# Performance work log

Hardware: AMD Instinct MI355X
Metric: run time of the kernel (lower is better)

The kernel has to match this reference:

```python
import jax, jax.numpy as jnp
import numpy as np
from jax import lax

# Module constraint: hidden_dim == state_dim == expand_dim (see broadcasting in original).
H = 128  # hidden_dim
N = 128  # state_dim
E = 128  # expand_dim = hidden_dim * expand_factor (expand_factor=1)
B, L = 4, 1024


def setup_inputs() -> dict:
    key = jax.random.key(0)
    ks = jax.random.split(key, 11)
    s = lambda fan: 1.0 / np.sqrt(fan)
    return {
        "u": jax.random.normal(ks[0], (B, L, H), jnp.float32),
        "W_in": jax.random.normal(ks[1], (H, 2 * E), jnp.float32) * s(H),
        "b_in": jax.random.normal(ks[2], (2 * E,), jnp.float32) * 0.01,
        "conv_w": jax.random.normal(ks[3], (E, 1, 3), jnp.float32) * s(3),
        "conv_b": jax.random.normal(ks[4], (E,), jnp.float32) * 0.01,
        "W_x": jax.random.normal(ks[5], (E, N + N + H), jnp.float32) * s(E),
        "b_x": jax.random.normal(ks[6], (N + N + H,), jnp.float32) * 0.01,
        "A_log": jax.random.normal(ks[7], (N,), jnp.float32),
        "D": jnp.ones((H,), jnp.float32),
        "W_out": jax.random.normal(ks[8], (E, H), jnp.float32) * s(E),
        "b_out": jax.random.normal(ks[9], (H,), jnp.float32) * 0.01,
    }


def reference(u, W_in, b_in, conv_w, conv_b, W_x, b_x, A_log, D, W_out, b_out):
    b, l, _ = u.shape
    xz = u @ W_in + b_in                       # [B,L,2E]
    x, z = jnp.split(xz, 2, axis=-1)           # [B,L,E] each
    # depthwise conv1d, kernel 3, padding 1 (groups == channels)
    xc = lax.conv_general_dilated(
        x.transpose(0, 2, 1), conv_w, window_strides=(1,), padding=[(1, 1)],
        feature_group_count=E, dimension_numbers=("NCH", "OIH", "NCH"))
    x = jax.nn.silu(xc.transpose(0, 2, 1) + conv_b)  # [B,L,E]
    ssm = x @ W_x + b_x                        # [B,L,2N+H]
    delta = jax.nn.softplus(ssm[..., :N])      # [B,L,N]
    Bm = ssm[..., N:2 * N]                     # [B,L,N]
    C = ssm[..., 2 * N:]                       # [B,L,H]
    A = -jnp.exp(A_log)                        # [N]

    def step(h, inp):
        d_t, B_t, C_t, x_t, u_t = inp          # [B,N],[B,N],[B,H],[B,E],[B,H]
        # A_discrete[b,t,i,j] = exp(delta[b,t,i] * A[j])  (outer broadcast, as in source)
        A_disc = jnp.exp(d_t[:, :, None] * A[None, None, :])       # [B,N,N]
        h = A_disc * h + (d_t * B_t)[:, :, None] * x_t[:, None, :]  # [B,N,E]
        y = (h * C_t[:, None, :]).sum(axis=1) + D * u_t             # [B,H]
        return h, y

    h0 = jnp.zeros((b, N, H), u.dtype)
    inputs = (delta.transpose(1, 0, 2), Bm.transpose(1, 0, 2),
              C.transpose(1, 0, 2), x.transpose(1, 0, 2), u.transpose(1, 0, 2))
    _, ys = lax.scan(step, h0, inputs)         # ys: [L,B,H]
    y = ys.transpose(1, 0, 2) * jax.nn.silu(z)  # [B,L,H] (E==H)
    return y @ W_out + b_out                   # dropout in eval mode: identity
```

## Files before the change

### kernel.cpp

```cpp
#include <hip/hip_runtime.h>
#include <hip/hip_bf16.h>

using bf16 = __hip_bfloat16;
typedef __attribute__((ext_vector_type(8))) short short8;
typedef __attribute__((ext_vector_type(4))) float f32x4;

#define BVAL 4
#define LVAL 1024
#define LOG2E 1.44269504f

#define TSEG 64
#define SSEG 16
#define JW 8
#define CH 16
#define PTS3 76

#define OFF_BIN    0
#define OFF_CONVW  256
#define OFF_CONVB  640
#define OFF_BX     768
#define OFF_ALOG   1152
#define OFF_D      1280
#define OFF_BOUT   1408
#define CVT_SMALL  1536

#define R_UBF   524288
#define R_WTIN  (R_UBF + 32768)
#define R_WTX   (R_WTIN + 49152)
#define R_WTOUT (R_WTX + 16384)
#define R_TOT   (R_WTOUT + CVT_SMALL)

__device__ __forceinline__ int dtype_flag(const void* D) {
    return ((*(const unsigned int*)D) & 0xFFFFu) != 0u ? 1 : 0;
}
__device__ __forceinline__ float ldin(const void* p, size_t i, int f) {
    return f ? __bfloat162float(((const bf16*)p)[i]) : ((const float*)p)[i];
}
__device__ __forceinline__ short f2bf(float x) {
    union { bf16 h; short s; } u; u.h = __float2bfloat16(x); return u.s;
}

__global__ void k0_cvt(const void* __restrict__ u, const void* __restrict__ W_in,
                       const void* __restrict__ b_in, const void* __restrict__ conv_w,
                       const void* __restrict__ conv_b, const void* __restrict__ W_x,
                       const void* __restrict__ b_x, const void* __restrict__ A_log,
                       const void* __restrict__ D, const void* __restrict__ W_out,
                       const void* __restrict__ b_out,
                       float* __restrict__ cvt, bf16* __restrict__ ubf,
                       bf16* __restrict__ wtin, bf16* __restrict__ wtx,
                       bf16* __restrict__ wtout) {
    int idx = blockIdx.x * 256 + threadIdx.x;
    if (idx >= R_TOT) return;
    int f = dtype_flag(D);
    if (idx < R_UBF) {
        ubf[idx] = __float2bfloat16(ldin(u, idx, f));
    } else if (idx < R_WTIN) {
        int rel = idx - R_UBF; int n = rel >> 7, k = rel & 127;
        wtin[rel] = __float2bfloat16(ldin(W_in, (size_t)k * 256 + n, f));
    } else if (idx < R_WTX) {
        int rel = idx - R_WTIN; int n = rel >> 7, k = rel & 127;
        wtx[rel] = __float2bfloat16(ldin(W_x, (size_t)k * 384 + n, f));
    } else if (idx < R_WTOUT) {
        int rel = idx - R_WTX; int n = rel >> 7, k = rel & 127;
        wtout[rel] = __float2bfloat16(ldin(W_out, (size_t)k * 128 + n, f));
    } else {
        int rel = idx - R_WTOUT; const void* p; int loc;
        if      (rel < 256)  { p = b_in;   loc = rel; }
        else if (rel < 640)  { p = conv_w; loc = rel - 256; }
        else if (rel < 768)  { p = conv_b; loc = rel - 640; }
        else if (rel < 1152) { p = b_x;    loc = rel - 768; }
        else if (rel < 1280) { p = A_log;  loc = rel - 1152; }
        else if (rel < 1408) { p = D;      loc = rel - 1280; }
        else                 { p = b_out;  loc = rel - 1408; }
        cvt[rel] = ldin(p, loc, f);
    }
}

__global__ void k1_mfma(const bf16* __restrict__ ubf, const bf16* __restrict__ wtin,
                        const float* __restrict__ cvt,
                        float* __restrict__ x_pre, float* __restrict__ zs) {
    int blk = blockIdx.x, mb = blk >> 3, cb = blk & 7;
    int tid = threadIdx.x, w = tid >> 6, lane = tid & 63;
    int quad = lane >> 4, sub = lane & 15;
    int m0 = mb * 64 + w * 16, c = cb * 16;
    f32x4 accX = {0.f, 0.f, 0.f, 0.f}, accZ = {0.f, 0.f, 0.f, 0.f};
    #pragma unroll
    for (int ks = 0; ks < 4; ++ks) {
        int k0 = ks * 32 + quad * 8;
        short8 a  = *(const short8*)(ubf + (size_t)(m0 + sub) * 128 + k0);
        short8 bX = *(const short8*)(wtin + (size_t)(c + sub) * 128 + k0);
        short8 bZ = *(const short8*)(wtin + (size_t)(128 + c + sub) * 128 + k0);
        accX = __builtin_amdgcn_mfma_f32_16x16x32_bf16(a, bX, accX, 0, 0, 0);
        accZ = __builtin_amdgcn_mfma_f32_16x16x32_bf16(a, bZ, accZ, 0, 0, 0);
    }
    int o = c + sub;
    float bx_ = cvt[OFF_BIN + o], bz_ = cvt[OFF_BIN + 128 + o];
    #pragma unroll
    for (int r = 0; r < 4; ++r) {
        int m = m0 + quad * 4 + r;
        float x = accX[r] + bx_;
        float z = accZ[r] + bz_;
        x_pre[(size_t)m * 128 + o] = x;
        zs[(size_t)m * 128 + o] = z / (1.0f + __expf(-z));
    }
}

__global__ void k3_mfma(const float* __restrict__ x_pre, const bf16* __restrict__ wtx,
                        const float* __restrict__ cvt, float* __restrict__ xs,
                        float* __restrict__ delta, float* __restrict__ dB,
                        float* __restrict__ Cc) {
    __shared__ float swc[128 * 4];
    int blk = blockIdx.x, mb = blk >> 3, cb = blk & 7;
    int tid = threadIdx.x, w = tid >> 6, lane = tid & 63;
    int quad = lane >> 4, sub = lane & 15;
    if (tid < 128) {
        swc[tid * 4 + 0] = cvt[OFF_CONVW + tid * 3 + 0];
        swc[tid * 4 + 1] = cvt[OFF_CONVW + tid * 3 + 1];
        swc[tid * 4 + 2] = cvt[OFF_CONVW + tid * 3 + 2];
        swc[tid * 4 + 3] = cvt[OFF_CONVB + tid];
    }
    __syncthreads();
    int m0 = mb * 64 + w * 16, c = cb * 16;
    int row = m0 + sub;
    int l = row & (LVAL - 1);
    const float* xr = x_pre + (size_t)row * 128;
    f32x4 accA = {0.f,0.f,0.f,0.f}, accB = {0.f,0.f,0.f,0.f}, accC = {0.f,0.f,0.f,0.f};
    #pragma unroll
    for (int ks = 0; ks < 4; ++ks) {
        int k0 = ks * 32 + quad * 8;
        float ccv[8], mmv[8], ppv[8];
        *(float4*)&ccv[0] = *(const float4*)(xr + k0);
        *(float4*)&ccv[4] = *(const float4*)(xr + k0 + 4);
        if (l > 0) {
            *(float4*)&mmv[0] = *(const float4*)(xr + k0 - 128);
            *(float4*)&mmv[4] = *(const float4*)(xr + k0 - 124);
        } else {
            #pragma unroll
            for (int i = 0; i < 8; ++i) mmv[i] = 0.f;
        }
        if (l < LVAL - 1) {
            *(float4*)&ppv[0] = *(const float4*)(xr + k0 + 128);
            *(float4*)&ppv[4] = *(const float4*)(xr + k0 + 132);
        } else {
            #pragma unroll
            for (int i = 0; i < 8; ++i) ppv[i] = 0.f;
        }
        float o[8];
        short8 a;
        #pragma unroll
        for (int i = 0; i < 8; ++i) {
            const float* wc = &swc[(k0 + i) * 4];
            float v = fmaf(wc[0], mmv[i], fmaf(wc[1], ccv[i], fmaf(wc[2], ppv[i], wc[3])));
            o[i] = v / (1.0f + __expf(-v));
            a[i] = f2bf(o[i]);
        }
        if (cb == 0) {
            *(float4*)(xs + (size_t)row * 128 + k0)     = *(float4*)&o[0];
            *(float4*)(xs + (size_t)row * 128 + k0 + 4) = *(float4*)&o[4];
        }
        short8 bA = *(const short8*)(wtx + (size_t)(c + sub) * 128 + k0);
        short8 bB = *(const short8*)(wtx + (size_t)(128 + c + sub) * 128 + k0);
        short8 bC = *(const short8*)(wtx + (size_t)(256 + c + sub) * 128 + k0);
        accA = __builtin_amdgcn_mfma_f32_16x16x32_bf16(a, bA, accA, 0, 0, 0);
        accB = __builtin_amdgcn_mfma_f32_16x16x32_bf16(a, bB, accB, 0, 0, 0);
        accC = __builtin_amdgcn_mfma_f32_16x16x32_bf16(a, bC, accC, 0, 0, 0);
    }
    int o = c + sub;
    float ba = cvt[OFF_BX + o], bb = cvt[OFF_BX + 128 + o], bc = cvt[OFF_BX + 256 + o];
    #pragma unroll
    for (int r = 0; r < 4; ++r) {
        int m = m0 + quad * 4 + r;
        size_t idx = (size_t)m * 128 + o;
        float d = accA[r] + ba;
        float sp = (d > 20.0f) ? d : log1pf(__expf(d));
        delta[idx] = sp;
        dB[idx] = sp * (accB[r] + bb);
        Cc[idx] = accC[r] + bc;
    }
}

__global__ __launch_bounds__(512, 8)
void k5a(const float* __restrict__ cvt, const float* __restrict__ delta,
         const float* __restrict__ dB, const float* __restrict__ xs,
         float* __restrict__ hout, float* __restrict__ Sd) {
    __shared__ float sdl[CH * 128], swl[CH * 128];
    __shared__ float sx[TSEG][JW];
    int blk = blockIdx.x;
    int b = blk >> 8, s = (blk >> 4) & 15, jg = blk & 15;
    int tid = threadIdx.x, w = tid >> 6, lane = tid & 63;
    int j = jg * JW + w;
    int t0 = s * TSEG;
    size_t base = (size_t)b * LVAL * 128;
    {
        int tt = tid >> 3, jj = tid & 7;
        sx[tt][jj] = xs[base + (size_t)(t0 + tt) * 128 + jg * JW + jj];
    }
    float a2 = -__expf(cvt[OFF_ALOG + j]) * LOG2E;
    float h0 = 0.f, h1 = 0.f, sd0 = 0.f, sd1 = 0.f;
    const float4* gd4 = (const float4*)(delta + base);
    const float4* gw4 = (const float4*)(dB + base);
    for (int c4 = 0; c4 < TSEG / CH; ++c4) {
        __syncthreads();
        int fb = (t0 + c4 * CH) * 32;
        ((float4*)sdl)[tid] = gd4[fb + tid];
        ((float4*)swl)[tid] = gw4[fb + tid];
        __syncthreads();
        #pragma unroll 8
        for (int k = 0; k < CH; ++k) {
            float2 dd = *(const float2*)&sdl[k * 128 + 2 * lane];
            float2 ww = *(const float2*)&swl[k * 128 + 2 * lane];
            float e0 = exp2f(dd.x * a2), e1 = exp2f(dd.y * a2);
            float xv = sx[c4 * CH + k][w];
            h0 = fmaf(e0, h0, ww.x * xv);
            h1 = fmaf(e1, h1, ww.y * xv);
            sd0 += dd.x; sd1 += dd.y;
        }
    }
    size_t cidx = (((size_t)(b * SSEG + s) * 128 + j) * 128) + 2 * lane;
    *(float2*)(hout + cidx) = make_float2(h0, h1);
    if (jg == 0 && w == 0) {
        *(float2*)(Sd + (size_t)(b * SSEG + s) * 128 + 2 * lane) = make_float2(sd0, sd1);
    }
}

__global__ void k5b(const float* __restrict__ cvt, const float* __restrict__ hout,
                    const float* __restrict__ Sd, float* __restrict__ hin) {
    int c = blockIdx.x * 2 + (threadIdx.x >> 6);
    int lane = threadIdx.x & 63;
    int b = c >> 7, j = c & 127;
    float a2 = -__expf(cvt[OFF_ALOG + j]) * LOG2E;
    float h0 = 0.f, h1 = 0.f;
    #pragma unroll
    for (int s = 0; s < SSEG; ++s) {
        size_t idx = (((size_t)(b * SSEG + s) * 128 + j) * 128) + 2 * lane;
        *(float2*)(hin + idx) = make_float2(h0, h1);
        float2 ho = *(const float2*)(hout + idx);
        float2 sd = *(const float2*)(Sd + (size_t)(b * SSEG + s) * 128 + 2 * lane);
        h0 = fmaf(exp2f(a2 * sd.x), h0, ho.x);
        h1 = fmaf(exp2f(a2 * sd.y), h1, ho.y);
    }
}

__global__ __launch_bounds__(512, 8)
void k5c(const float* __restrict__ cvt, const float* __restrict__ delta,
         const float* __restrict__ dB, const float* __restrict__ Cc,
         const float* __restrict__ xs, const float* __restrict__ zs,
         const float* __restrict__ hin, const void* __restrict__ uin,
         const void* __restrict__ Din, bf16* __restrict__ y2bf) {
    __shared__ float sdl[CH * 128], swl[CH * 128];
    __shared__ float sx[TSEG][JW];
    __shared__ float pt[JW][8 * PTS3];
    int blk = blockIdx.x;
    int b = blk >> 8, s = (blk >> 4) & 15, jg = blk & 15;
    int tid = threadIdx.x, w = tid >> 6, lane = tid & 63;
    int j = jg * JW + w;
    int t0 = s * TSEG;
    size_t base = (size_t)b * LVAL * 128;
    int f = dtype_flag(Din);
    {
        int tt = tid >> 3, jj = tid & 7;
        sx[tt][jj] = xs[base + (size_t)(t0 + tt) * 128 + jg * JW + jj];
    }
    float a2 = -__expf(cvt[OFF_ALOG + j]) * LOG2E;
    float Dj = cvt[OFF_D + j];
    size_t cidx = (((size_t)(b * SSEG + s) * 128 + j) * 128) + 2 * lane;
    float2 hh = *(const float2*)(hin + cidx);
    float h0 = hh.x, h1 = hh.y;
    const float4* gd4 = (const float4*)(delta + base);
    const float4* gw4 = (const float4*)(dB + base);
    float* ptw = pt[w];
    int t_r = lane >> 3, g8 = lane & 7;
    for (int c4 = 0; c4 < TSEG / CH; ++c4) {
        __syncthreads();
        int fb = (t0 + c4 * CH) * 32;
        ((float4*)sdl)[tid] = gd4[fb + tid];
        ((float4*)swl)[tid] = gw4[fb + tid];
        __syncthreads();
        for (int cb = 0; cb < CH / 8; ++cb) {
            int tte = c4 * CH + cb * 8 + t_r;
            size_t gi = base + (size_t)(t0 + tte) * 128 + j;
            float cC = Cc[gi];
            float cz = zs[gi];
            float cu = ldin(uin, gi, f);
            #pragma unroll
            for (int k = 0; k < 8; ++k) {
                int kk = cb * 8 + k;
                float2 dd = *(const float2*)&sdl[kk * 128 + 2 * lane];
                float2 ww = *(const float2*)&swl[kk * 128 + 2 * lane];
                float xv = sx[c4 * CH + kk][w];
                h0 = fmaf(exp2f(dd.x * a2), h0, ww.x * xv);
                h1 = fmaf(exp2f(dd.y * a2), h1, ww.y * xv);
                ptw[k * PTS3 + lane] = h0 + h1;
            }
            const float4* pr = (const float4*)&ptw[t_r * PTS3 + g8 * 8];
            float4 v0 = pr[0], v1 = pr[1];
            float sum = ((v0.x + v0.y) + (v0.z + v0.w)) + ((v1.x + v1.y) + (v1.z + v1.w));
            sum += __shfl_xor(sum, 1, 64);
            sum += __shfl_xor(sum, 2, 64);
            sum += __shfl_xor(sum, 4, 64);
            if (g8 == 0) {
                float y = fmaf(cC, sum, Dj * cu);
                y2bf[gi] = __float2bfloat16(y * cz);
            }
        }
    }
}

__global__ void k6_mfma(const bf16* __restrict__ y2bf, const bf16* __restrict__ wtout,
                        const float* __restrict__ cvt, const void* __restrict__ Din,
                        void* __restrict__ out) {
    int blk = blockIdx.x, mb = blk >> 2, nb = blk & 3;
    int tid = threadIdx.x, w = tid >> 6, lane = tid & 63;
    int quad = lane >> 4, sub = lane & 15;
    int m0 = mb * 64 + w * 16, n0 = nb * 32;
    f32x4 acc0 = {0.f,0.f,0.f,0.f}, acc1 = {0.f,0.f,0.f,0.f};
    #pragma unroll
    for (int ks = 0; ks < 4; ++ks) {
        int k0 = ks * 32 + quad * 8;
        short8 a  = *(const short8*)(y2bf + (size_t)(m0 + sub) * 128 + k0);
        short8 b0 = *(const short8*)(wtout + (size_t)(n0 + sub) * 128 + k0);
        short8 b1 = *(const short8*)(wtout + (size_t)(n0 + 16 + sub) * 128 + k0);
        acc0 = __builtin_amdgcn_mfma_f32_16x16x32_bf16(a, b0, acc0, 0, 0, 0);
        acc1 = __builtin_amdgcn_mfma_f32_16x16x32_bf16(a, b1, acc1, 0, 0, 0);
    }
    int f = dtype_flag(Din);
    float bo0 = cvt[OFF_BOUT + n0 + sub], bo1 = cvt[OFF_BOUT + n0 + 16 + sub];
    #pragma unroll
    for (int r = 0; r < 4; ++r) {
        int m = m0 + quad * 4 + r;
        float v0 = acc0[r] + bo0, v1 = acc1[r] + bo1;
        if (f) {
            ((bf16*)out)[(size_t)m * 128 + n0 + sub] = __float2bfloat16(v0);
            ((bf16*)out)[(size_t)m * 128 + n0 + 16 + sub] = __float2bfloat16(v1);
        } else {
            ((float*)out)[(size_t)m * 128 + n0 + sub] = v0;
            ((float*)out)[(size_t)m * 128 + n0 + 16 + sub] = v1;
        }
    }
}

extern "C" void kernel_launch(void* const* d_in, const int* in_sizes, int n_in,
                              void* d_out, int out_size, void* d_ws, size_t ws_size,
                              hipStream_t stream) {
    const size_t NE = (size_t)BVAL * LVAL * 128;
    const size_t NC = (size_t)BVAL * SSEG * 128 * 128;

    float* cvt   = (float*)d_ws;
    float* bufs  = cvt + 2048;
    float* x_pre = bufs + 0 * NE;
    float* zs    = bufs + 1 * NE;
    float* xs    = bufs + 2 * NE;
    float* delta = bufs + 3 * NE;
    float* dB    = bufs + 4 * NE;
    float* Cc    = bufs + 5 * NE;
    float* hout  = bufs + 6 * NE;
    float* hin   = hout + NC;
    float* Sd    = hin + NC;
    bf16* ubf    = (bf16*)(Sd + 8192);
    bf16* y2bf   = ubf + NE;
    bf16* wtin   = y2bf + NE;
    bf16* wtx    = wtin + 32768;
    bf16* wtout  = wtx + 49152;

    k0_cvt<<<(R_TOT + 255) / 256, 256, 0, stream>>>(
        d_in[0], d_in[1], d_in[2], d_in[3], d_in[4], d_in[5],
        d_in[6], d_in[7], d_in[8], d_in[9], d_in[10],
        cvt, ubf, wtin, wtx, wtout);
    k1_mfma<<<512, 256, 0, stream>>>(ubf, wtin, cvt, x_pre, zs);
    k3_mfma<<<512, 256, 0, stream>>>(x_pre, wtx, cvt, xs, delta, dB, Cc);
    k5a<<<BVAL * SSEG * (128 / JW), 512, 0, stream>>>(cvt, delta, dB, xs, hout, Sd);
    k5b<<<256, 128, 0, stream>>>(cvt, hout, Sd, hin);
    k5c<<<BVAL * SSEG * (128 / JW), 512, 0, stream>>>(cvt, delta, dB, Cc, xs, zs, hin,
        d_in[0], d_in[8], y2bf);
    k6_mfma<<<256, 256, 0, stream>>>(y2bf, wtout, cvt, d_in[8], d_out);
}
```

Before: 153.2 us.

## Replace chunked three-pass scan with single sequential scan split over state halves

Replaces the three-kernel segmented scan (local scan, carry propagation, rescan with output) with one sequential scan kernel over the full sequence. Each block handles one batch and 8 columns for half of the state dimension, with double-buffered prefetch of delta/dB/x into shared memory. Per-half partial C·h sums go to two buffers, and the D*u skip term, gating by z and the bf16 cast move into the output GEMM's A-operand load. This removes the second scan pass and the carry kernel, but leaves only 128 blocks, each running a 1024-step serial chain.

```diff
diff --git a/kernel.cpp b/kernel.cpp
--- a/kernel.cpp
+++ b/kernel.cpp
@@ -9,11 +9,9 @@
 #define LVAL 1024
 #define LOG2E 1.44269504f
 
-#define TSEG 64
-#define SSEG 16
-#define JW 8
-#define CH 16
-#define PTS3 76
+#define SCH 16
+#define NCHUNK (LVAL / SCH)
+#define PTS 68
 
 #define OFF_BIN    0
 #define OFF_CONVW  256
@@ -179,151 +177,116 @@
     }
 }
 
-__global__ __launch_bounds__(512, 8)
-void k5a(const float* __restrict__ cvt, const float* __restrict__ delta,
-         const float* __restrict__ dB, const float* __restrict__ xs,
-         float* __restrict__ hout, float* __restrict__ Sd) {
-    __shared__ float sdl[CH * 128], swl[CH * 128];
-    __shared__ float sx[TSEG][JW];
+__global__ __launch_bounds__(512)
+void k5_scan(const float* __restrict__ cvt, const float* __restrict__ delta,
+             const float* __restrict__ dB, const float* __restrict__ xs,
+             const float* __restrict__ Cc, float* __restrict__ pP0) {
+    __shared__ float sd[2][SCH][64];
+    __shared__ float sw[2][SCH][64];
+    __shared__ float sxc[2][SCH][8];
+    __shared__ float spt[8][8 * PTS];
+    const size_t NEc = (size_t)BVAL * LVAL * 128;
     int blk = blockIdx.x;
-    int b = blk >> 8, s = (blk >> 4) & 15, jg = blk & 15;
+    int half = blk & 1, jg = (blk >> 1) & 15, b = blk >> 5;
     int tid = threadIdx.x, w = tid >> 6, lane = tid & 63;
-    int j = jg * JW + w;
-    int t0 = s * TSEG;
+    int j = jg * 8 + w;
     size_t base = (size_t)b * LVAL * 128;
-    {
-        int tt = tid >> 3, jj = tid & 7;
-        sx[tt][jj] = xs[base + (size_t)(t0 + tt) * 128 + jg * JW + jj];
-    }
+    float* __restrict__ pP = pP0 + (size_t)half * NEc;
     float a2 = -__expf(cvt[OFF_ALOG + j]) * LOG2E;
-    float h0 = 0.f, h1 = 0.f, sd0 = 0.f, sd1 = 0.f;
     const float4* gd4 = (const float4*)(delta + base);
     const float4* gw4 = (const float4*)(dB + base);
-    for (int c4 = 0; c4 < TSEG / CH; ++c4) {
-        __syncthreads();
-        int fb = (t0 + c4 * CH) * 32;
-        ((float4*)sdl)[tid] = gd4[fb + tid];
-        ((float4*)swl)[tid] = gw4[fb + tid];
-        __syncthreads();
-        #pragma unroll 8
-        for (int k = 0; k < CH; ++k) {
-            float2 dd = *(const float2*)&sdl[k * 128 + 2 * lane];
-            float2 ww = *(const float2*)&swl[k * 128 + 2 * lane];
-            float e0 = exp2f(dd.x * a2), e1 = exp2f(dd.y * a2);
-            float xv = sx[c4 * CH + k][w];
-            h0 = fmaf(e0, h0, ww.x * xv);
-            h1 = fmaf(e1, h1, ww.y * xv);
-            sd0 += dd.x; sd1 += dd.y;
-        }
-    }
-    size_t cidx = (((size_t)(b * SSEG + s) * 128 + j) * 128) + 2 * lane;
-    *(float2*)(hout + cidx) = make_float2(h0, h1);
-    if (jg == 0 && w == 0) {
-        *(float2*)(Sd + (size_t)(b * SSEG + s) * 128 + 2 * lane) = make_float2(sd0, sd1);
-    }
-}
-
-__global__ void k5b(const float* __restrict__ cvt, const float* __restrict__ hout,
-                    const float* __restrict__ Sd, float* __restrict__ hin) {
-    int c = blockIdx.x * 2 + (threadIdx.x >> 6);
-    int lane = threadIdx.x & 63;
-    int b = c >> 7, j = c & 127;
-    float a2 = -__expf(cvt[OFF_ALOG + j]) * LOG2E;
-    float h0 = 0.f, h1 = 0.f;
-    #pragma unroll
-    for (int s = 0; s < SSEG; ++s) {
-        size_t idx = (((size_t)(b * SSEG + s) * 128 + j) * 128) + 2 * lane;
-        *(float2*)(hin + idx) = make_float2(h0, h1);
-        float2 ho = *(const float2*)(hout + idx);
-        float2 sd = *(const float2*)(Sd + (size_t)(b * SSEG + s) * 128 + 2 * lane);
-        h0 = fmaf(exp2f(a2 * sd.x), h0, ho.x);
-        h1 = fmaf(exp2f(a2 * sd.y), h1, ho.y);
-    }
-}
-
-__global__ __launch_bounds__(512, 8)
-void k5c(const float* __restrict__ cvt, const float* __restrict__ delta,
-         const float* __restrict__ dB, const float* __restrict__ Cc,
-         const float* __restrict__ xs, const float* __restrict__ zs,
-         const float* __restrict__ hin, const void* __restrict__ uin,
-         const void* __restrict__ Din, bf16* __restrict__ y2bf) {
-    __shared__ float sdl[CH * 128], swl[CH * 128];
-    __shared__ float sx[TSEG][JW];
-    __shared__ float pt[JW][8 * PTS3];
-    int blk = blockIdx.x;
-    int b = blk >> 8, s = (blk >> 4) & 15, jg = blk & 15;
-    int tid = threadIdx.x, w = tid >> 6, lane = tid & 63;
-    int j = jg * JW + w;
-    int t0 = s * TSEG;
-    size_t base = (size_t)b * LVAL * 128;
-    int f = dtype_flag(Din);
+    int st = (tid & 255) >> 4, sq = tid & 15;
     {
-        int tt = tid >> 3, jj = tid & 7;
-        sx[tt][jj] = xs[base + (size_t)(t0 + tt) * 128 + jg * JW + jj];
-    }
-    float a2 = -__expf(cvt[OFF_ALOG + j]) * LOG2E;
-    float Dj = cvt[OFF_D + j];
-    size_t cidx = (((size_t)(b * SSEG + s) * 128 + j) * 128) + 2 * lane;
-    float2 hh = *(const float2*)(hin + cidx);
-    float h0 = hh.x, h1 = hh.y;
-    const float4* gd4 = (const float4*)(delta + base);
-    const float4* gw4 = (const float4*)(dB + base);
-    float* ptw = pt[w];
+        float4 v;
+        if (tid < 256) v = gd4[st * 32 + half * 16 + sq];
+        else           v = gw4[st * 32 + half * 16 + sq];
+        if (tid < 256) *(float4*)&sd[0][st][sq * 4] = v;
+        else           *(float4*)&sw[0][st][sq * 4] = v;
+        if (tid < 128) sxc[0][tid >> 3][tid & 7] =
+            xs[base + (size_t)(tid >> 3) * 128 + jg * 8 + (tid & 7)];
+    }
+    __syncthreads();
+    float h = 0.f;
+    float* ptw = spt[w];
     int t_r = lane >> 3, g8 = lane & 7;
-    for (int c4 = 0; c4 < TSEG / CH; ++c4) {
-        __syncthreads();
-        int fb = (t0 + c4 * CH) * 32;
-        ((float4*)sdl)[tid] = gd4[fb + tid];
-        ((float4*)swl)[tid] = gw4[fb + tid];
-        __syncthreads();
-        for (int cb = 0; cb < CH / 8; ++cb) {
-            int tte = c4 * CH + cb * 8 + t_r;
-            size_t gi = base + (size_t)(t0 + tte) * 128 + j;
-            float cC = Cc[gi];
-            float cz = zs[gi];
-            float cu = ldin(uin, gi, f);
+    for (int c = 0; c < NCHUNK; ++c) {
+        int cur = c & 1, nxt = cur ^ 1;
+        float4 pf_a; float pf_x;
+        bool more = (c + 1 < NCHUNK);
+        if (more) {
+            int cn = c + 1;
+            if (tid < 256) pf_a = gd4[(cn * SCH + st) * 32 + half * 16 + sq];
+            else           pf_a = gw4[(cn * SCH + st) * 32 + half * 16 + sq];
+            if (tid < 128) pf_x = xs[base + (size_t)(cn * SCH + (tid >> 3)) * 128
+                                     + jg * 8 + (tid & 7)];
+        }
+        #pragma unroll
+        for (int cb = 0; cb < 2; ++cb) {
             #pragma unroll
             for (int k = 0; k < 8; ++k) {
                 int kk = cb * 8 + k;
-                float2 dd = *(const float2*)&sdl[kk * 128 + 2 * lane];
-                float2 ww = *(const float2*)&swl[kk * 128 + 2 * lane];
-                float xv = sx[c4 * CH + kk][w];
-                h0 = fmaf(exp2f(dd.x * a2), h0, ww.x * xv);
-                h1 = fmaf(exp2f(dd.y * a2), h1, ww.y * xv);
-                ptw[k * PTS3 + lane] = h0 + h1;
+                float dd = sd[cur][kk][lane];
+                float ww = sw[cur][kk][lane];
+                float xv = sxc[cur][kk][w];
+                h = fmaf(exp2f(dd * a2), h, ww * xv);
+                ptw[k * PTS + lane] = h;
             }
-            const float4* pr = (const float4*)&ptw[t_r * PTS3 + g8 * 8];
+            const float4* pr = (const float4*)&ptw[t_r * PTS + g8 * 8];
             float4 v0 = pr[0], v1 = pr[1];
             float sum = ((v0.x + v0.y) + (v0.z + v0.w)) + ((v1.x + v1.y) + (v1.z + v1.w));
             sum += __shfl_xor(sum, 1, 64);
             sum += __shfl_xor(sum, 2, 64);
             sum += __shfl_xor(sum, 4, 64);
             if (g8 == 0) {
-                float y = fmaf(cC, sum, Dj * cu);
-                y2bf[gi] = __float2bfloat16(y * cz);
+                size_t gi = base + (size_t)(c * SCH + cb * 8 + t_r) * 128 + j;
+                pP[gi] = Cc[gi] * sum;
             }
         }
-    }
-}
-
-__global__ void k6_mfma(const bf16* __restrict__ y2bf, const bf16* __restrict__ wtout,
-                        const float* __restrict__ cvt, const void* __restrict__ Din,
-                        void* __restrict__ out) {
+        if (more) {
+            if (tid < 256) *(float4*)&sd[nxt][st][sq * 4] = pf_a;
+            else           *(float4*)&sw[nxt][st][sq * 4] = pf_a;
+            if (tid < 128) sxc[nxt][tid >> 3][tid & 7] = pf_x;
+        }
+        __syncthreads();
+    }
+}
+
+__global__ void k6_mfma(const float* __restrict__ pA, const float* __restrict__ pB,
+                        const float* __restrict__ zs, const void* __restrict__ uin,
+                        const bf16* __restrict__ wtout, const float* __restrict__ cvt,
+                        const void* __restrict__ Din, void* __restrict__ out) {
     int blk = blockIdx.x, mb = blk >> 2, nb = blk & 3;
     int tid = threadIdx.x, w = tid >> 6, lane = tid & 63;
     int quad = lane >> 4, sub = lane & 15;
     int m0 = mb * 64 + w * 16, n0 = nb * 32;
+    int f = dtype_flag(Din);
+    int row = m0 + sub;
     f32x4 acc0 = {0.f,0.f,0.f,0.f}, acc1 = {0.f,0.f,0.f,0.f};
     #pragma unroll
     for (int ks = 0; ks < 4; ++ks) {
         int k0 = ks * 32 + quad * 8;
-        short8 a  = *(const short8*)(y2bf + (size_t)(m0 + sub) * 128 + k0);
+        size_t ri = (size_t)row * 128 + k0;
+        float av[8], bv[8], zv[8], dv[8];
+        *(float4*)&av[0] = *(const float4*)(pA + ri);
+        *(float4*)&av[4] = *(const float4*)(pA + ri + 4);
+        *(float4*)&bv[0] = *(const float4*)(pB + ri);
+        *(float4*)&bv[4] = *(const float4*)(pB + ri + 4);
+        *(float4*)&zv[0] = *(const float4*)(zs + ri);
+        *(float4*)&zv[4] = *(const float4*)(zs + ri + 4);
+        *(float4*)&dv[0] = *(const float4*)(cvt + OFF_D + k0);
+        *(float4*)&dv[4] = *(const float4*)(cvt + OFF_D + k0 + 4);
+        short8 a;
+        #pragma unroll
+        for (int i = 0; i < 8; ++i) {
+            float uu = ldin(uin, ri + i, f);
+            float v = (av[i] + bv[i] + dv[i] * uu) * zv[i];
+            a[i] = f2bf(v);
+        }
         short8 b0 = *(const short8*)(wtout + (size_t)(n0 + sub) * 128 + k0);
         short8 b1 = *(const short8*)(wtout + (size_t)(n0 + 16 + sub) * 128 + k0);
         acc0 = __builtin_amdgcn_mfma_f32_16x16x32_bf16(a, b0, acc0, 0, 0, 0);
         acc1 = __builtin_amdgcn_mfma_f32_16x16x32_bf16(a, b1, acc1, 0, 0, 0);
     }
-    int f = dtype_flag(Din);
     float bo0 = cvt[OFF_BOUT + n0 + sub], bo1 = cvt[OFF_BOUT + n0 + 16 + sub];
     #pragma unroll
     for (int r = 0; r < 4; ++r) {
@@ -343,7 +306,6 @@
                               void* d_out, int out_size, void* d_ws, size_t ws_size,
                               hipStream_t stream) {
     const size_t NE = (size_t)BVAL * LVAL * 128;
-    const size_t NC = (size_t)BVAL * SSEG * 128 * 128;
 
     float* cvt   = (float*)d_ws;
     float* bufs  = cvt + 2048;
@@ -353,12 +315,9 @@
     float* delta = bufs + 3 * NE;
     float* dB    = bufs + 4 * NE;
     float* Cc    = bufs + 5 * NE;
-    float* hout  = bufs + 6 * NE;
-    float* hin   = hout + NC;
-    float* Sd    = hin + NC;
-    bf16* ubf    = (bf16*)(Sd + 8192);
-    bf16* y2bf   = ubf + NE;
-    bf16* wtin   = y2bf + NE;
+    float* pA    = bufs + 6 * NE;
+    bf16* ubf    = (bf16*)(bufs + 8 * NE);
+    bf16* wtin   = ubf + NE;
     bf16* wtx    = wtin + 32768;
     bf16* wtout  = wtx + 49152;
 
@@ -368,9 +327,7 @@
         cvt, ubf, wtin, wtx, wtout);
     k1_mfma<<<512, 256, 0, stream>>>(ubf, wtin, cvt, x_pre, zs);
     k3_mfma<<<512, 256, 0, stream>>>(x_pre, wtx, cvt, xs, delta, dB, Cc);
-    k5a<<<BVAL * SSEG * (128 / JW), 512, 0, stream>>>(cvt, delta, dB, xs, hout, Sd);
-    k5b<<<256, 128, 0, stream>>>(cvt, hout, Sd, hin);
-    k5c<<<BVAL * SSEG * (128 / JW), 512, 0, stream>>>(cvt, delta, dB, Cc, xs, zs, hin,
-        d_in[0], d_in[8], y2bf);
-    k6_mfma<<<256, 256, 0, stream>>>(y2bf, wtout, cvt, d_in[8], d_out);
-}
+    k5_scan<<<128, 512, 0, stream>>>(cvt, delta, dB, xs, Cc, pA);
+    k6_mfma<<<256, 256, 0, stream>>>(pA, pA + NE, zs, d_in[0], wtout, cvt,
+                                     d_in[8], d_out);
+}
```

New measurement: 211.5 us. 1.38x slower.
